# Performance work log

Hardware: AMD Instinct MI355X
Metric: run time of the kernel (lower is better)

## Reference

```python
import jax, jax.numpy as jnp
import numpy as np

PAD = 0  # padding_index
BIG = 10000.0

B, S = 1024, 128
V, E, H, T = 200, 512, 512, 24


def setup_inputs() -> dict:
    key = jax.random.key(0)
    ks = jax.random.split(key, 12)
    sequences = jax.random.randint(ks[0], (B, S), 0, V, dtype=jnp.int32)
    labels = jax.random.randint(ks[1], (B, S), 0, T, dtype=jnp.int32)
    true_lengths = jax.random.randint(ks[2], (B,), 1, S, dtype=jnp.int32)
    emb = jax.random.normal(ks[3], (V, E), dtype=jnp.float32) * 0.1
    emb = emb.at[PAD].set(0.0)  # nn.Embedding padding_idx zeros that row
    w1 = jax.random.normal(ks[4], (H, H), dtype=jnp.float32) * (1.0 / np.sqrt(H))
    b1 = jax.random.normal(ks[5], (H,), dtype=jnp.float32) * 0.01
    w2 = jax.random.normal(ks[6], (T, H), dtype=jnp.float32) * (1.0 / np.sqrt(H))
    b2 = jax.random.normal(ks[7], (T,), dtype=jnp.float32) * 0.01
    start_trans = jax.random.uniform(ks[8], (T,), jnp.float32, -0.1, 0.1)
    end_trans = jax.random.uniform(ks[9], (T,), jnp.float32, -0.1, 0.1)
    transitions = jax.random.uniform(ks[10], (T, T), jnp.float32, -0.1, 0.1)
    return {"sequences": sequences, "labels": labels, "true_lengths": true_lengths,
            "emb": emb, "w1": w1, "b1": b1, "w2": w2, "b2": b2,
            "start_trans": start_trans, "end_trans": end_trans, "transitions": transitions}


def _emissions(sequences, emb, w1, b1, w2, b2):
    pad_mask = (sequences == PAD).astype(jnp.float32)  # [B,S]
    x = emb[sequences]                                  # [B,S,E]
    h = jax.nn.relu(x @ w1.T + b1)                      # [B,S,H]
    scores = jax.nn.relu(h @ w2.T + b2)                 # [B,S,T]
    scores = scores.at[:, :, PAD].add(pad_mask * BIG)
    return scores


def _crf_nll_mean(emissions, labels, start_trans, end_trans, transitions):
    # emissions [B,S,T], labels [B,S]; mask = all ones (none passed in forward)
    # numerator: score of gold path
    em_gold = jnp.take_along_axis(emissions, labels[..., None], axis=2)[..., 0]  # [B,S]
    num = (start_trans[labels[:, 0]]
           + em_gold.sum(axis=1)
           + transitions[labels[:, :-1], labels[:, 1:]].sum(axis=1)
           + end_trans[labels[:, -1]])  # [B]
    # denominator: forward algorithm via scan over time
    em_t = jnp.swapaxes(emissions, 0, 1)  # [S,B,T]
    alpha0 = start_trans[None, :] + em_t[0]  # [B,T]

    def step(alpha, emit):
        # alpha [B,T_prev], transitions [T_prev,T_next], emit [B,T_next]
        nxt = jax.nn.logsumexp(alpha[:, :, None] + transitions[None] + emit[:, None, :], axis=1)
        return nxt, None

    alpha, _ = jax.lax.scan(step, alpha0, em_t[1:])
    denom = jax.nn.logsumexp(alpha + end_trans[None, :], axis=1)  # [B]
    llh = num - denom
    return -jnp.mean(llh)


def reference(sequences, labels, true_lengths, emb, w1, b1, w2, b2,
              start_trans, end_trans, transitions):
    emissions = _emissions(sequences, emb, w1, b1, w2, b2)
    return _crf_nll_mean(emissions, labels, start_trans, end_trans, transitions)
```

## Files before the change

### kernel.cpp

```cpp
#include <hip/hip_runtime.h>
#include <math.h>

#define PAD_IDX 0
#define BIGV 10000.0f
constexpr int B_ = 1024, S_ = 128, V_ = 200, E_ = 512, H_ = 512, T_ = 24;

constexpr int OFF_H  = 262144;
constexpr int OFF_EM = 364544;
constexpr int OFF_W  = 369344;
constexpr int OFF_MX = 374144;

typedef __attribute__((ext_vector_type(8)))  short    bf8frag;
typedef __attribute__((ext_vector_type(16))) float    facc16;
typedef __attribute__((ext_vector_type(4)))  unsigned u32x4;

__device__ __forceinline__ unsigned pkbf(float lo, float hi) {
    const unsigned a = __float_as_uint(lo), b = __float_as_uint(hi);
    return ((a + 0x8000u) >> 16) | ((b + 0x8000u) & 0xffff0000u);
}

__global__ __launch_bounds__(256) void mlp1_kernel(
    const float* __restrict__ emb, const float* __restrict__ w1,
    const float* __restrict__ b1, float* __restrict__ h_ws,
    float* __restrict__ out)
{
    __shared__ unsigned w1b[256][32];
    __shared__ unsigned embb[256][32];
    __shared__ float    part[4][64][17];
    const int tid = threadIdx.x;
    const int vt = blockIdx.x % 7, tt = blockIdx.x / 7;
    const int v0 = vt * 32, t0 = tt * 32;

    if (blockIdx.x == 0 && tid == 0) out[0] = 0.f;

    {
        const int row = tid >> 3;
        const int seg = tid & 7;
        {
            const float* __restrict__ src = w1 + (size_t)(t0 + row) * E_ + seg * 64;
            #pragma unroll
            for (int i = 0; i < 16; ++i) {
                const float4 f = *(const float4*)(src + i * 4);
                const int kp = seg * 32 + i * 2;
                w1b[kp][row]     = pkbf(f.x, f.y);
                w1b[kp + 1][row] = pkbf(f.z, f.w);
            }
        }
        const int v = v0 + row;
        if (v < V_) {
            const float* __restrict__ src = emb + (size_t)v * E_ + seg * 64;
            #pragma unroll
            for (int i = 0; i < 16; ++i) {
                const float4 f = *(const float4*)(src + i * 4);
                const int kp = seg * 32 + i * 2;
                embb[kp][row]     = pkbf(f.x, f.y);
                embb[kp + 1][row] = pkbf(f.z, f.w);
            }
        } else {
            #pragma unroll
            for (int i = 0; i < 16; ++i) {
                const int kp = seg * 32 + i * 2;
                embb[kp][row] = 0u; embb[kp + 1][row] = 0u;
            }
        }
    }
    __syncthreads();

    {
        const int wave = tid >> 6, lane = tid & 63;
        const int mn = lane & 31, h2 = lane >> 5;
        facc16 acc;
        #pragma unroll
        for (int r = 0; r < 16; ++r) acc[r] = 0.f;
        #pragma unroll
        for (int c = 0; c < 8; ++c) {
            const int kp = wave * 64 + c * 8 + 4 * h2;
            u32x4 Af, Bf;
            #pragma unroll
            for (int r = 0; r < 4; ++r) {
                Af[r] = embb[kp + r][mn];
                Bf[r] = w1b[kp + r][mn];
            }
            acc = __builtin_amdgcn_mfma_f32_32x32x16_bf16(
                      __builtin_bit_cast(bf8frag, Af),
                      __builtin_bit_cast(bf8frag, Bf), acc, 0, 0, 0);
        }
        #pragma unroll
        for (int r = 0; r < 16; ++r) part[wave][lane][r] = acc[r];
    }
    __syncthreads();

    {
        const int l = tid & 63, rg = tid >> 6;
        const int col = l & 31, hh = l >> 5;
        const float bb = b1[t0 + col];
        #pragma unroll
        for (int i = 0; i < 4; ++i) {
            const int r = rg * 4 + i;
            const float s = (part[0][l][r] + part[1][l][r])
                          + (part[2][l][r] + part[3][l][r]);
            const int vrow = (r & 3) + 8 * (r >> 2) + 4 * hh;
            const int v = v0 + vrow;
            if (v < V_)
                h_ws[(size_t)v * H_ + t0 + col] = fmaxf(s + bb, 0.f);
        }
    }
}

__global__ __launch_bounds__(256) void emis_kernel(
    const float* __restrict__ h_ws, const float* __restrict__ w2,
    const float* __restrict__ b2, float* __restrict__ em_table,
    float* __restrict__ w_table, float* __restrict__ emax_arr)
{
    __shared__ float em_row[32];
    const int v = blockIdx.x;
    const int t = threadIdx.x;
    const int wave = t >> 6, lane = t & 63;
    const float* __restrict__ hrow = h_ws + (size_t)v * H_;
    for (int jj2 = 0; jj2 < 6; ++jj2) {
        const int jo = wave * 6 + jj2;
        float part = 0.f;
        #pragma unroll
        for (int m = 0; m < H_ / 64; ++m) {
            const int k = lane + m * 64;
            part = fmaf(hrow[k], w2[(size_t)jo * H_ + k], part);
        }
        #pragma unroll
        for (int off = 32; off; off >>= 1)
            part += __shfl_xor(part, off, 64);
        if (lane == 0) {
            float val = fmaxf(part + b2[jo], 0.f);
            if (v == 0 && jo == PAD_IDX) val += BIGV;
            em_row[jo] = val;
        }
    }
    __syncthreads();
    if (t < 32) {
        float x = (t < T_) ? em_row[t] : -INFINITY;
        float mx = x;
        #pragma unroll
        for (int off = 16; off; off >>= 1)
            mx = fmaxf(mx, __shfl_xor(mx, off, 32));
        if (t < T_) {
            em_table[v * T_ + t] = x;
            w_table[v * T_ + t]  = __expf(x - mx);
        }
        if (t == 0) emax_arr[v] = mx;
    }
}

__global__ __launch_bounds__(256) void crf_kernel(
    const int* __restrict__ seq, const int* __restrict__ labels,
    const float* __restrict__ start_t, const float* __restrict__ end_t,
    const float* __restrict__ trans, const float* __restrict__ em_table,
    const float* __restrict__ w_table, const float* __restrict__ emax_arr,
    float* __restrict__ out)
{
    __shared__ __align__(16) float w_s[V_ * T_];
    __shared__ int   tok_s[S_ * 32];
    __shared__ float meet_s[64 * 12];
    __shared__ float logb_s[64];
    __shared__ float gp_s[32];
    const int tid = threadIdx.x;
    const int g = blockIdx.x;

    for (int i = tid; i < V_ * T_ / 4; i += 256)
        ((float4*)w_s)[i] = ((const float4*)w_table)[i];
    {
        const int bq = tid & 31, c = tid >> 5;
        const int* __restrict__ src = seq + (size_t)(g * 32 + bq) * S_ + c * 16;
        #pragma unroll
        for (int i = 0; i < 16; ++i)
            tok_s[(c * 16 + i) * 32 + bq] = src[i];
    }
    if (tid < 32) gp_s[tid] = 0.f;
    __syncthreads();

    if (tid < 128) {
        const bool isF = (tid < 64);
        const int lane = tid & 63;
        const int n = lane & 31;
        const int h = lane >> 5;

        u32x4 A1p, A2p;
        {
            float a1e[8], a2e[8];
            #pragma unroll
            for (int j = 0; j < 8; ++j) {
                const int k1 = 8 * h + j;
                const int k2 = 16 + 8 * h + j;
                float v1 = 0.f, v2 = 0.f;
                if (n < T_) {
                    v1 = __expf(isF ? trans[k1 * T_ + n] : trans[n * T_ + k1]);
                    if (k2 < T_)
                        v2 = __expf(isF ? trans[k2 * T_ + n] : trans[n * T_ + k2]);
                }
                a1e[j] = v1; a2e[j] = v2;
            }
            #pragma unroll
            for (int r = 0; r < 4; ++r) {
                A1p[r] = pkbf(a1e[2 * r], a1e[2 * r + 1]);
                A2p[r] = pkbf(a2e[2 * r], a2e[2 * r + 1]);
            }
        }

        float logacc;
        u32x4 B1p, B2p;
        {
            const int tokI = tok_s[(isF ? 0 : (S_ - 1)) * 32 + n];
            float q1[8], q2[8];
            if (isF) {
                float e1[8], e2[8];
                #pragma unroll
                for (int j = 0; j < 8; ++j) { e1[j] = 0.f; e2[j] = 0.f; }
                float mx = -INFINITY;
                #pragma unroll
                for (int j = 0; j < 8; ++j) {
                    const int r1 = 8 * h + j;
                    e1[j] = start_t[r1] + em_table[tokI * T_ + r1];
                    mx = fmaxf(mx, e1[j]);
                }
                if (h == 0) {
                    #pragma unroll
                    for (int j = 0; j < 8; ++j) {
                        const int r2 = 16 + j;
                        e2[j] = start_t[r2] + em_table[tokI * T_ + r2];
                        mx = fmaxf(mx, e2[j]);
                    }
                }
                mx = fmaxf(mx, __shfl_xor(mx, 32, 64));
                #pragma unroll
                for (int j = 0; j < 8; ++j) {
                    q1[j] = __expf(e1[j] - mx);
                    q2[j] = (h == 0) ? __expf(e2[j] - mx) : 0.f;
                }
                logacc = mx;
            } else {
                #pragma unroll
                for (int j = 0; j < 8; ++j) {
                    const int r1 = 8 * h + j;
                    q1[j] = w_s[tokI * T_ + r1] * __expf(end_t[r1]);
                    const int r2 = 16 + j;
                    q2[j] = (h == 0) ? w_s[tokI * T_ + r2] * __expf(end_t[r2]) : 0.f;
                }
                logacc = 0.f;
            }
            #pragma unroll
            for (int r = 0; r < 4; ++r) {
                B1p[r] = pkbf(q1[2 * r], q1[2 * r + 1]);
                B2p[r] = pkbf(q2[2 * r], q2[2 * r + 1]);
            }
        }

        const int dir  = isF ? 1 : -1;
        const int offi = isF ? 1 : (S_ - 2);

        float4 Wc0, Wc1, Wc2;
        {
            const int tk = tok_s[offi * 32 + n];
            const float* wb = w_s + tk * T_ + 4 * h;
            Wc0 = *(const float4*)(wb);
            Wc1 = *(const float4*)(wb + 8);
            Wc2 = *(const float4*)(wb + 16);
        }

        float d[12];
        for (int s = 1; s <= 63; ++s) {
            const int sn = (s < 63) ? (s + 1) : 63;
            const int tkN = tok_s[(offi + dir * (sn - 1)) * 32 + n];
            const float* wbn = w_s + tkN * T_ + 4 * h;
            const float4 Wn0 = *(const float4*)(wbn);
            const float4 Wn1 = *(const float4*)(wbn + 8);
            const float4 Wn2 = *(const float4*)(wbn + 16);

            facc16 accA, accB;
            #pragma unroll
            for (int r = 0; r < 16; ++r) { accA[r] = 0.f; accB[r] = 0.f; }
            accA = __builtin_amdgcn_mfma_f32_32x32x16_bf16(
                       __builtin_bit_cast(bf8frag, A1p),
                       __builtin_bit_cast(bf8frag, B1p), accA, 0, 0, 0);
            accB = __builtin_amdgcn_mfma_f32_32x32x16_bf16(
                       __builtin_bit_cast(bf8frag, A2p),
                       __builtin_bit_cast(bf8frag, B2p), accB, 0, 0, 0);

            d[0]  = (accA[0]  + accB[0] ) * Wc0.x;
            d[1]  = (accA[1]  + accB[1] ) * Wc0.y;
            d[2]  = (accA[2]  + accB[2] ) * Wc0.z;
            d[3]  = (accA[3]  + accB[3] ) * Wc0.w;
            d[4]  = (accA[4]  + accB[4] ) * Wc1.x;
            d[5]  = (accA[5]  + accB[5] ) * Wc1.y;
            d[6]  = (accA[6]  + accB[6] ) * Wc1.z;
            d[7]  = (accA[7]  + accB[7] ) * Wc1.w;
            d[8]  = (accA[8]  + accB[8] ) * Wc2.x;
            d[9]  = (accA[9]  + accB[9] ) * Wc2.y;
            d[10] = (accA[10] + accB[10]) * Wc2.z;
            d[11] = (accA[11] + accB[11]) * Wc2.w;

            if ((s & 15) == 0 || s == 63) {
                float mx = d[0];
                #pragma unroll
                for (int r = 1; r < 12; ++r) mx = fmaxf(mx, d[r]);
                mx = fmaxf(mx, __shfl_xor(mx, 32, 64));
                const float inv = 1.0f / mx;
                #pragma unroll
                for (int r = 0; r < 12; ++r) d[r] *= inv;
                logacc += __logf(mx);
            }

            const unsigned P0 = pkbf(d[0], d[1]),  P1 = pkbf(d[2], d[3]);
            const unsigned P2 = pkbf(d[4], d[5]),  P3 = pkbf(d[6], d[7]);
            const unsigned P4 = pkbf(d[8], d[9]),  P5 = pkbf(d[10], d[11]);
            const unsigned XP0 = (unsigned)__shfl_xor((int)P0, 32, 64);
            const unsigned XP1 = (unsigned)__shfl_xor((int)P1, 32, 64);
            const unsigned XP2 = (unsigned)__shfl_xor((int)P2, 32, 64);
            const unsigned XP3 = (unsigned)__shfl_xor((int)P3, 32, 64);
            const unsigned XP4 = (unsigned)__shfl_xor((int)P4, 32, 64);
            const unsigned XP5 = (unsigned)__shfl_xor((int)P5, 32, 64);
            B1p[0] = h ? XP2 : P0;  B1p[1] = h ? XP3 : P1;
            B1p[2] = h ? P2  : XP0; B1p[3] = h ? P3  : XP1;
            B2p[0] = h ? 0u  : P4;  B2p[1] = h ? 0u  : P5;
            B2p[2] = h ? 0u  : XP4; B2p[3] = h ? 0u  : XP5;

            Wc0 = Wn0; Wc1 = Wn1; Wc2 = Wn2;
        }

        if (!isF) {
            #pragma unroll
            for (int r = 0; r < 12; ++r) meet_s[lane * 12 + r] = d[r];
            logb_s[lane] = logacc;
        }
        __syncthreads();
        if (isF) {
            facc16 accA, accB;
            #pragma unroll
            for (int r = 0; r < 16; ++r) { accA[r] = 0.f; accB[r] = 0.f; }
            accA = __builtin_amdgcn_mfma_f32_32x32x16_bf16(
                       __builtin_bit_cast(bf8frag, A1p),
                       __builtin_bit_cast(bf8frag, B1p), accA, 0, 0, 0);
            accB = __builtin_amdgcn_mfma_f32_32x32x16_bf16(
                       __builtin_bit_cast(bf8frag, A2p),
                       __builtin_bit_cast(bf8frag, B2p), accB, 0, 0, 0);
            float dot = 0.f;
            #pragma unroll
            for (int r = 0; r < 12; ++r)
                dot = fmaf(accA[r] + accB[r], meet_s[lane * 12 + r], dot);
            dot += __shfl_xor(dot, 32, 64);
            const float denom = logacc + logb_s[lane] + __logf(dot);
            float val = 0.f;
            if (h == 0)
                val = (denom - gp_s[n]) * (1.0f / (float)B_);
            #pragma unroll
            for (int off = 32; off; off >>= 1)
                val += __shfl_xor(val, off, 64);
            if (lane == 0) atomicAdd(out, val);
        }
    } else {
        const int t2 = tid - 128;
        const int n = t2 & 31;
        const int r = t2 >> 5;
        const int b = g * 32 + n;
        const int* __restrict__ lrow = labels + (size_t)b * S_;
        float gp = 0.f;
        for (int i = 0; i < 32; ++i) {
            const int s = r * 32 + i;
            const int tk = tok_s[s * 32 + n];
            const int ls = lrow[s];
            gp += em_table[tk * T_ + ls];
            if (s >= 1) gp -= emax_arr[tk];
            if (s < S_ - 1) gp += trans[ls * T_ + lrow[s + 1]];
            if (s == 0) gp += start_t[ls];
            if (s == S_ - 1) gp += end_t[ls];
        }
        atomicAdd(&gp_s[n], gp);
        __syncthreads();
    }
}

extern "C" void kernel_launch(void* const* d_in, const int* in_sizes, int n_in,
                              void* d_out, int out_size, void* d_ws, size_t ws_size,
                              hipStream_t stream) {
    const int*   seq     = (const int*)d_in[0];
    const int*   labels  = (const int*)d_in[1];
    const float* emb     = (const float*)d_in[3];
    const float* w1      = (const float*)d_in[4];
    const float* b1      = (const float*)d_in[5];
    const float* w2      = (const float*)d_in[6];
    const float* b2      = (const float*)d_in[7];
    const float* start_t = (const float*)d_in[8];
    const float* end_t   = (const float*)d_in[9];
    const float* trans   = (const float*)d_in[10];

    float* ws            = (float*)d_ws;
    float* h_ws          = ws + OFF_H;
    float* em_table      = ws + OFF_EM;
    float* w_table       = ws + OFF_W;
    float* emax_arr      = ws + OFF_MX;
    float* out           = (float*)d_out;

    mlp1_kernel<<<112, 256, 0, stream>>>(emb, w1, b1, h_ws, out);
    emis_kernel<<<V_, 256, 0, stream>>>(h_ws, w2, b2, em_table, w_table, emax_arr);
    crf_kernel<<<B_ / 32, 256, 0, stream>>>(seq, labels, start_t, end_t, trans,
                                            em_table, w_table, emax_arr, out);
}
```

Before: 108.9 us.

## Compute emission table with bf16 MFMA over 8 vocab rows per block

The emission kernel now handles 8 vocabulary rows per block instead of one. It stages h and w2 into shared memory as packed bf16 and computes the 8x24 projection with 32x32x16 bf16 MFMA instructions, splitting K across the four waves and reducing the partial sums in LDS. This replaces 200 blocks of scalar dot products with shuffle reductions and cuts redundant w2 reads. In exchange it adds bf16 rounding to the emissions and wastes most of the MFMA tile, since only 8 of 32 rows and 24 of 32 columns are used.

New measurement: 110.9 us. Within noise of the previous version (+1.8%).

```diff
diff --git a/kernel.cpp b/kernel.cpp
--- a/kernel.cpp
+++ b/kernel.cpp
@@ -112,40 +112,102 @@
     const float* __restrict__ b2, float* __restrict__ em_table,
     float* __restrict__ w_table, float* __restrict__ emax_arr)
 {
-    __shared__ float em_row[32];
-    const int v = blockIdx.x;
-    const int t = threadIdx.x;
-    const int wave = t >> 6, lane = t & 63;
-    const float* __restrict__ hrow = h_ws + (size_t)v * H_;
-    for (int jj2 = 0; jj2 < 6; ++jj2) {
-        const int jo = wave * 6 + jj2;
-        float part = 0.f;
-        #pragma unroll
-        for (int m = 0; m < H_ / 64; ++m) {
-            const int k = lane + m * 64;
-            part = fmaf(hrow[k], w2[(size_t)jo * H_ + k], part);
-        }
-        #pragma unroll
-        for (int off = 32; off; off >>= 1)
-            part += __shfl_xor(part, off, 64);
-        if (lane == 0) {
-            float val = fmaxf(part + b2[jo], 0.f);
-            if (v == 0 && jo == PAD_IDX) val += BIGV;
-            em_row[jo] = val;
-        }
-    }
-    __syncthreads();
-    if (t < 32) {
-        float x = (t < T_) ? em_row[t] : -INFINITY;
-        float mx = x;
-        #pragma unroll
-        for (int off = 16; off; off >>= 1)
-            mx = fmaxf(mx, __shfl_xor(mx, off, 32));
-        if (t < T_) {
-            em_table[v * T_ + t] = x;
-            w_table[v * T_ + t]  = __expf(x - mx);
-        }
-        if (t == 0) emax_arr[v] = mx;
+    __shared__ unsigned hA[256][32];
+    __shared__ unsigned w2B[256][32];
+    __shared__ float    part[4][64][5];
+    __shared__ float    em_t[8][33];
+    __shared__ float    mx_s[8];
+    const int tid = threadIdx.x;
+    const int v0 = blockIdx.x * 8;
+
+    {
+        const int row = tid >> 5;
+        const int seg = tid & 31;
+        const float* __restrict__ src = h_ws + (size_t)(v0 + row) * H_ + seg * 16;
+        #pragma unroll
+        for (int i = 0; i < 4; ++i) {
+            const float4 f = *(const float4*)(src + i * 4);
+            const int kp = seg * 8 + i * 2;
+            hA[kp][row]     = pkbf(f.x, f.y);
+            hA[kp + 1][row] = pkbf(f.z, f.w);
+        }
+        for (int idx = tid; idx < 256 * 24; idx += 256) {
+            const int kp = idx / 24, rz = 8 + idx % 24;
+            hA[kp][rz] = 0u;
+        }
+    }
+    {
+        if (tid < 192) {
+            const int row = tid >> 3;
+            const int seg = tid & 7;
+            const float* __restrict__ src = w2 + (size_t)row * H_ + seg * 64;
+            #pragma unroll
+            for (int i = 0; i < 16; ++i) {
+                const float4 f = *(const float4*)(src + i * 4);
+                const int kp = seg * 32 + i * 2;
+                w2B[kp][row]     = pkbf(f.x, f.y);
+                w2B[kp + 1][row] = pkbf(f.z, f.w);
+            }
+        }
+        for (int idx = tid; idx < 256 * 8; idx += 256) {
+            const int kp = idx >> 3, cz = 24 + (idx & 7);
+            w2B[kp][cz] = 0u;
+        }
+    }
+    __syncthreads();
+
+    {
+        const int wave = tid >> 6, lane = tid & 63;
+        const int mn = lane & 31, h2 = lane >> 5;
+        facc16 acc;
+        #pragma unroll
+        for (int r = 0; r < 16; ++r) acc[r] = 0.f;
+        #pragma unroll
+        for (int c = 0; c < 8; ++c) {
+            const int kp = wave * 64 + c * 8 + 4 * h2;
+            u32x4 Af, Bf;
+            #pragma unroll
+            for (int r = 0; r < 4; ++r) {
+                Af[r] = hA[kp + r][mn];
+                Bf[r] = w2B[kp + r][mn];
+            }
+            acc = __builtin_amdgcn_mfma_f32_32x32x16_bf16(
+                      __builtin_bit_cast(bf8frag, Af),
+                      __builtin_bit_cast(bf8frag, Bf), acc, 0, 0, 0);
+        }
+        #pragma unroll
+        for (int r = 0; r < 4; ++r) part[wave][lane][r] = acc[r];
+    }
+    __syncthreads();
+
+    if (tid < 64) {
+        const int col = tid & 31, h2 = tid >> 5;
+        #pragma unroll
+        for (int r = 0; r < 4; ++r) {
+            const float s = (part[0][tid][r] + part[1][tid][r])
+                          + (part[2][tid][r] + part[3][tid][r]);
+            const int vrow = r + 4 * h2;
+            if (col < T_) {
+                float val = fmaxf(s + b2[col], 0.f);
+                if (v0 == 0 && vrow == 0 && col == PAD_IDX) val += BIGV;
+                em_t[vrow][col] = val;
+            }
+        }
+    }
+    __syncthreads();
+    if (tid < 8) {
+        float mx = em_t[tid][0];
+        #pragma unroll
+        for (int c = 1; c < T_; ++c) mx = fmaxf(mx, em_t[tid][c]);
+        mx_s[tid] = mx;
+        emax_arr[v0 + tid] = mx;
+    }
+    __syncthreads();
+    if (tid < 8 * T_) {
+        const int r = tid / T_, c = tid % T_;
+        const float em = em_t[r][c];
+        em_table[v0 * T_ + tid] = em;
+        w_table[v0 * T_ + tid]  = __expf(em - mx_s[r]);
     }
 }
 
@@ -398,7 +460,7 @@
     float* out           = (float*)d_out;
 
     mlp1_kernel<<<112, 256, 0, stream>>>(emb, w1, b1, h_ws, out);
-    emis_kernel<<<V_, 256, 0, stream>>>(h_ws, w2, b2, em_table, w_table, emax_arr);
+    emis_kernel<<<V_ / 8, 256, 0, stream>>>(h_ws, w2, b2, em_table, w_table, emax_arr);
     crf_kernel<<<B_ / 32, 256, 0, stream>>>(seq, labels, start_t, end_t, trans,
                                             em_table, w_table, emax_arr, out);
 }
```
